# Performance work log

Hardware: AMD Instinct MI355X
Metric: run time of the kernel (lower is better)

The kernel has to match this reference:

```python
import jax, jax.numpy as jnp
import numpy as np


def setup_inputs() -> dict:
    key = jax.random.key(0)
    kx, kf = jax.random.split(key)
    x = jax.random.normal(kx, (1, 3, 512, 512), dtype=jnp.float32)
    # per-pixel 9x9 kernels; normalize each to sum to 1 like a PSF
    kernel_field = jax.random.uniform(kf, (512, 512, 9, 9), dtype=jnp.float32)
    kernel_field = kernel_field / jnp.sum(kernel_field, axis=(-2, -1), keepdims=True)
    return {"x": x, "kernel_field": kernel_field}


def reference(x, kernel_field):
    """Spatially varying blur: out[b,c,h,w] = sum_{i,j} x_pad[b,c,h+i,w+j] * K[h,w,i,j].

    Equivalent to the torch unfold + einsum('bckhw,khw->bchw') but computed as a
    fused shift-multiply-accumulate over the kH*kW offsets, avoiding the
    (B,C,kH*kW,H,W) im2col blowup.
    """
    B, C, H, W = x.shape
    kH, kW = kernel_field.shape[2], kernel_field.shape[3]
    pad = kH // 2
    xp = jnp.pad(x, ((0, 0), (0, 0), (pad, pad), (pad, pad)), mode="reflect")
    out = jnp.zeros_like(x)
    for i in range(kH):          # small fixed loop over kernel taps (81)
        for j in range(kW):
            out = out + xp[:, :, i:i + H, j:j + W] * kernel_field[:, :, i, j]
    return out
```

## Files before the change

kernel.cpp:

```cpp
#include <hip/hip_runtime.h>

#define H 512
#define W 512
#define KH 9
#define KW 9
#define PAD 4
#define BX 16
#define BY 16
#define TS (BX + KW - 1)

__device__ __forceinline__ int reflect_idx(int p, int n) {
    if (p < 0) p = -p;
    if (p >= n) p = 2 * n - 2 - p;
    return p;
}

__global__ __launch_bounds__(BX * BY) void svblur_kernel(
    const float* __restrict__ x,
    const float* __restrict__ kf,
    float* __restrict__ out)
{
    __shared__ float xs[3][TS][TS];

    const int tx = threadIdx.x;
    const int ty = threadIdx.y;
    const int tid = ty * BX + tx;
    const int w0 = blockIdx.x * BX;
    const int h0 = blockIdx.y * BY;

    for (int idx = tid; idx < TS * TS; idx += BX * BY) {
        int r = idx / TS;
        int c = idx - r * TS;
        int gh = reflect_idx(h0 - PAD + r, H);
        int gw = reflect_idx(w0 - PAD + c, W);
        int g = gh * W + gw;
        xs[0][r][c] = x[g];
        xs[1][r][c] = x[H * W + g];
        xs[2][r][c] = x[2 * H * W + g];
    }
    __syncthreads();

    const int h = h0 + ty;
    const int w = w0 + tx;
    const float* kp = kf + (size_t)(h * W + w) * (KH * KW);

    float a0 = 0.f, a1 = 0.f, a2 = 0.f;
#pragma unroll
    for (int i = 0; i < KH; ++i) {
#pragma unroll
        for (int j = 0; j < KW; ++j) {
            float wgt = kp[i * KW + j];
            a0 += xs[0][ty + i][tx + j] * wgt;
            a1 += xs[1][ty + i][tx + j] * wgt;
            a2 += xs[2][ty + i][tx + j] * wgt;
        }
    }

    const int o = h * W + w;
    out[o] = a0;
    out[H * W + o] = a1;
    out[2 * H * W + o] = a2;
}

extern "C" void kernel_launch(void* const* d_in, const int* in_sizes, int n_in,
                              void* d_out, int out_size, void* d_ws, size_t ws_size,
                              hipStream_t stream) {
    const float* x  = (const float*)d_in[0];
    const float* kf = (const float*)d_in[1];
    float* out = (float*)d_out;

    dim3 block(BX, BY);
    dim3 grid(W / BX, H / BY);
    svblur_kernel<<<grid, block, 0, stream>>>(x, kf, out);
}
```

Before: 29.27 us.

## Stage kernel weights and image rows into LDS via direct global-to-LDS loads

Replaces the 16x16 2D tile with one 64-lane wavefront per 64-pixel row segment. Each pixel's 81 weights are copied contiguously into LDS with 16-byte global_load_lds transfers, so the read is coalesced instead of each lane striding 324 bytes apart. The 9 reflected input rows for all 3 channels are also staged through global_load_lds. In exchange, halo reuse shrinks: each block reloads 9 input rows for a single output row. The kernel also relies on a low-level builtin and its LDS write ordering.

```diff
diff --git a/kernel.cpp b/kernel.cpp
--- a/kernel.cpp
+++ b/kernel.cpp
@@ -1,62 +1,92 @@
 #include <hip/hip_runtime.h>
+#include <stdint.h>
 
 #define H 512
 #define W 512
-#define KH 9
-#define KW 9
+#define KT 81
 #define PAD 4
-#define BX 16
-#define BY 16
-#define TS (BX + KW - 1)
+#define SEGW 64
+#define TSW (SEGW + 2 * PAD)
+#define XROWS 9
+#define XDWORDS (3 * XROWS * TSW)
 
-__device__ __forceinline__ int reflect_idx(int p, int n) {
+typedef const __attribute__((address_space(1))) void* gptr1_t;
+typedef __attribute__((address_space(3))) void* lptr3_t;
+
+__device__ __forceinline__ int reflect_idx(int p) {
     if (p < 0) p = -p;
-    if (p >= n) p = 2 * n - 2 - p;
+    if (p >= H) p = 2 * H - 2 - p;
     return p;
 }
 
-__global__ __launch_bounds__(BX * BY) void svblur_kernel(
+__global__ __launch_bounds__(64) void svblur_kernel(
     const float* __restrict__ x,
     const float* __restrict__ kf,
     float* __restrict__ out)
 {
-    __shared__ float xs[3][TS][TS];
+    __shared__ float wlds[SEGW * KT];
+    __shared__ float xlds[3][XROWS][TSW];
 
-    const int tx = threadIdx.x;
-    const int ty = threadIdx.y;
-    const int tid = ty * BX + tx;
-    const int w0 = blockIdx.x * BX;
-    const int h0 = blockIdx.y * BY;
+    const int lane = (int)threadIdx.x;
+    const int bid = (int)blockIdx.x;
+    const int h  = bid >> 3;
+    const int w0 = (bid & 7) * SEGW;
 
-    for (int idx = tid; idx < TS * TS; idx += BX * BY) {
-        int r = idx / TS;
-        int c = idx - r * TS;
-        int gh = reflect_idx(h0 - PAD + r, H);
-        int gw = reflect_idx(w0 - PAD + c, W);
-        int g = gh * W + gw;
-        xs[0][r][c] = x[g];
-        xs[1][r][c] = x[H * W + g];
-        xs[2][r][c] = x[2 * H * W + g];
-    }
-    __syncthreads();
-
-    const int h = h0 + ty;
-    const int w = w0 + tx;
-    const float* kp = kf + (size_t)(h * W + w) * (KH * KW);
-
-    float a0 = 0.f, a1 = 0.f, a2 = 0.f;
+    {
+        const uint32_t* wsrc = (const uint32_t*)(kf + (size_t)(h * W + w0) * KT);
+        char* wbase = (char*)&wlds[0];
 #pragma unroll
-    for (int i = 0; i < KH; ++i) {
-#pragma unroll
-        for (int j = 0; j < KW; ++j) {
-            float wgt = kp[i * KW + j];
-            a0 += xs[0][ty + i][tx + j] * wgt;
-            a1 += xs[1][ty + i][tx + j] * wgt;
-            a2 += xs[2][ty + i][tx + j] * wgt;
+        for (int it = 0; it < 20; ++it) {
+            __builtin_amdgcn_global_load_lds(
+                (gptr1_t)(wsrc + it * 256 + lane * 4),
+                (lptr3_t)(wbase + it * 1024),
+                16, 0, 0);
+        }
+        if (lane < 16) {
+            __builtin_amdgcn_global_load_lds(
+                (gptr1_t)(wsrc + 20 * 256 + lane * 4),
+                (lptr3_t)(wbase + 20 * 1024),
+                16, 0, 0);
         }
     }
 
-    const int o = h * W + w;
+    {
+        const uint32_t* xsrc = (const uint32_t*)x;
+        char* xbase = (char*)&xlds[0][0][0];
+#pragma unroll
+        for (int it = 0; it < 31; ++it) {
+            int idx = it * 64 + lane;
+            if (idx < XDWORDS) {
+                int c   = idx / (XROWS * TSW);
+                int rem = idx - c * (XROWS * TSW);
+                int r   = rem / TSW;
+                int col = rem - r * TSW;
+                int gh = reflect_idx(h - PAD + r);
+                int gw = reflect_idx(w0 - PAD + col);
+                __builtin_amdgcn_global_load_lds(
+                    (gptr1_t)(xsrc + (size_t)c * H * W + gh * W + gw),
+                    (lptr3_t)(xbase + it * 256),
+                    4, 0, 0);
+            }
+        }
+    }
+
+    __syncthreads();
+
+    const float* wp = &wlds[lane * KT];
+    float a0 = 0.f, a1 = 0.f, a2 = 0.f;
+#pragma unroll
+    for (int i = 0; i < 9; ++i) {
+#pragma unroll
+        for (int j = 0; j < 9; ++j) {
+            float wv = wp[i * 9 + j];
+            a0 += xlds[0][i][lane + j] * wv;
+            a1 += xlds[1][i][lane + j] * wv;
+            a2 += xlds[2][i][lane + j] * wv;
+        }
+    }
+
+    const int o = h * W + w0 + lane;
     out[o] = a0;
     out[H * W + o] = a1;
     out[2 * H * W + o] = a2;
@@ -69,7 +99,7 @@
     const float* kf = (const float*)d_in[1];
     float* out = (float*)d_out;
 
-    dim3 block(BX, BY);
-    dim3 grid(W / BX, H / BY);
+    dim3 block(64);
+    dim3 grid(H * (W / SEGW));
     svblur_kernel<<<grid, block, 0, stream>>>(x, kf, out);
 }
```

Result: faster. 28.29 us (-3.3%).

## Stage per-pixel kernels through LDS with coalesced float4 loads, read image directly

Applied to the files above, without the earlier changes.

Each 64-thread block now handles one row segment of 64 pixels. It first copies those pixels' 81-tap kernels into LDS with coalesced float4 loads, replacing the strided per-thread kernel reads. The input image is no longer tiled into shared memory; each thread reads its 9x9 neighbourhood from global memory through cache, with reflect indices precomputed. This targets the dominant kernel-field bandwidth cost. In exchange, image reads become redundant global and cache loads, and the LDS footprint is about 20KB per block, which may cap occupancy.

```diff
diff --git a/kernel.cpp b/kernel.cpp
--- a/kernel.cpp
+++ b/kernel.cpp
@@ -1,65 +1,76 @@
 #include <hip/hip_runtime.h>
+#include <stdint.h>
 
 #define H 512
 #define W 512
-#define KH 9
-#define KW 9
+#define HW (H * W)
+#define KT 81
 #define PAD 4
-#define BX 16
-#define BY 16
-#define TS (BX + KW - 1)
 
-__device__ __forceinline__ int reflect_idx(int p, int n) {
+__device__ __forceinline__ int reflect_idx(int p) {
     if (p < 0) p = -p;
-    if (p >= n) p = 2 * n - 2 - p;
+    if (p >= H) p = 2 * H - 2 - p;
     return p;
 }
 
-__global__ __launch_bounds__(BX * BY) void svblur_kernel(
+__global__ __launch_bounds__(64) void svblur_kernel(
     const float* __restrict__ x,
     const float* __restrict__ kf,
     float* __restrict__ out)
 {
-    __shared__ float xs[3][TS][TS];
+    __shared__ float wlds[64 * KT];
 
-    const int tx = threadIdx.x;
-    const int ty = threadIdx.y;
-    const int tid = ty * BX + tx;
-    const int w0 = blockIdx.x * BX;
-    const int h0 = blockIdx.y * BY;
+    const int l   = (int)threadIdx.x;
+    const int bid = (int)blockIdx.x;
+    const int h   = bid >> 3;
+    const int w0  = (bid & 7) << 6;
 
-    for (int idx = tid; idx < TS * TS; idx += BX * BY) {
-        int r = idx / TS;
-        int c = idx - r * TS;
-        int gh = reflect_idx(h0 - PAD + r, H);
-        int gw = reflect_idx(w0 - PAD + c, W);
-        int g = gh * W + gw;
-        xs[0][r][c] = x[g];
-        xs[1][r][c] = x[H * W + g];
-        xs[2][r][c] = x[2 * H * W + g];
+    {
+        const float4* ws = (const float4*)(kf + ((size_t)h * W + w0) * KT);
+        float4* wd = (float4*)wlds;
+#pragma unroll
+        for (int it = 0; it < 20; ++it)
+            wd[it * 64 + l] = ws[it * 64 + l];
+        if (l < 16)
+            wd[20 * 64 + l] = ws[20 * 64 + l];
     }
-    __syncthreads();
 
-    const int h = h0 + ty;
-    const int w = w0 + tx;
-    const float* kp = kf + (size_t)(h * W + w) * (KH * KW);
+    int rgw[9];
+#pragma unroll
+    for (int j = 0; j < 9; ++j)
+        rgw[j] = reflect_idx(w0 - PAD + l + j);
 
+    const float* wp = wlds + l * KT;
     float a0 = 0.f, a1 = 0.f, a2 = 0.f;
+
 #pragma unroll
-    for (int i = 0; i < KH; ++i) {
+    for (int i = 0; i < 9; ++i) {
+        const int gh = reflect_idx(h - PAD + i);
+        const float* r0 = x + (size_t)gh * W;
+        const float* r1 = r0 + HW;
+        const float* r2 = r1 + HW;
+
+        float xv0[9], xv1[9], xv2[9];
 #pragma unroll
-        for (int j = 0; j < KW; ++j) {
-            float wgt = kp[i * KW + j];
-            a0 += xs[0][ty + i][tx + j] * wgt;
-            a1 += xs[1][ty + i][tx + j] * wgt;
-            a2 += xs[2][ty + i][tx + j] * wgt;
+        for (int j = 0; j < 9; ++j) {
+            xv0[j] = r0[rgw[j]];
+            xv1[j] = r1[rgw[j]];
+            xv2[j] = r2[rgw[j]];
+        }
+
+#pragma unroll
+        for (int j = 0; j < 9; ++j) {
+            const float wv = wp[i * 9 + j];
+            a0 = fmaf(xv0[j], wv, a0);
+            a1 = fmaf(xv1[j], wv, a1);
+            a2 = fmaf(xv2[j], wv, a2);
         }
     }
 
-    const int o = h * W + w;
-    out[o] = a0;
-    out[H * W + o] = a1;
-    out[2 * H * W + o] = a2;
+    const int o = h * W + w0 + l;
+    out[o]          = a0;
+    out[o + HW]     = a1;
+    out[o + 2 * HW] = a2;
 }
 
 extern "C" void kernel_launch(void* const* d_in, const int* in_sizes, int n_in,
@@ -69,7 +80,7 @@
     const float* kf = (const float*)d_in[1];
     float* out = (float*)d_out;
 
-    dim3 block(BX, BY);
-    dim3 grid(W / BX, H / BY);
+    dim3 block(64);
+    dim3 grid(H * (W / 64));
     svblur_kernel<<<grid, block, 0, stream>>>(x, kf, out);
 }
```

Result: faster. 26.66 us (-8.9%).
